# Kernel tuning notes

Hardware: AMD Instinct MI355X
Metric: run time of the kernel (lower is better)

## Reference

```python
import jax, jax.numpy as jnp
import numpy as np

KH = KW = 9
BN_EPS = 1e-5


def conv3x3(x, w):
    # x: [B,Cin,H,W], w: [Cout,Cin,3,3], stride 1, padding 1
    return jax.lax.conv_general_dilated(
        x, w, window_strides=(1, 1), padding=((1, 1), (1, 1)),
        dimension_numbers=("NCHW", "OIHW", "NCHW"))


def cbr(x, w, bn):
    # bn: [4, C] rows = (gamma, beta, running_mean, running_var); inference-mode BN
    g, b, m, v = bn[0], bn[1], bn[2], bn[3]
    x = conv3x3(x, w)
    x = (x - m[:, None, None]) * (g[:, None, None] / jnp.sqrt(v[:, None, None] + BN_EPS)) + b[:, None, None]
    return jax.nn.relu(x)


def weighting(x, atten):
    # x: [B,C,H,W], atten: [B,H,W,KH*KW]
    # out[b,c,h,w] = sum_k atten[b,h,w,k] * x[b,c, h+dh(k), w+dw(k)]  (zero-padded window)
    B, C, H, W = x.shape
    patches = jax.lax.conv_general_dilated_patches(
        x, filter_shape=(KH, KW), window_strides=(1, 1),
        padding=((KH // 2, KH // 2), (KW // 2, KW // 2)))  # [B, C*KH*KW, H, W], channel-major
    patches = patches.reshape(B, C, KH * KW, H, W)
    return jnp.einsum("bckhw,bhwk->bchw", patches, atten)


def _make_params(key, fc_dim=1024):
    d4, d16 = fc_dim // 4, fc_dim // 16
    ks = jax.random.split(key, 16)
    def conv_w(k, co, ci):
        return jax.random.normal(k, (co, ci, 3, 3), jnp.float32) * (1.0 / np.sqrt(ci * 9))
    def bn(k, c):
        g = 1.0 + 0.1 * jax.random.normal(k, (c,), jnp.float32)
        return jnp.stack([g, jnp.zeros((c,)), jnp.zeros((c,)), jnp.ones((c,))])
    p = {}
    p["w1"], p["bn1"] = conv_w(ks[0], d4, fc_dim), bn(ks[1], d4)
    p["w2"], p["bn2"] = conv_w(ks[2], d16, d4), bn(ks[3], d16)
    p["w3"], p["bn3"] = conv_w(ks[4], d4, d16), bn(ks[5], d4)
    p["w4"], p["bn4"] = conv_w(ks[6], d4, fc_dim), bn(ks[7], d4)
    p["w5"], p["bn5"] = conv_w(ks[8], d4, d4), bn(ks[9], d4)
    p["fw1"] = jax.random.normal(ks[10], (10, d4), jnp.float32) * (1.0 / np.sqrt(d4))
    p["fb1"] = jnp.zeros((10,), jnp.float32)
    p["fw2"] = jax.random.normal(ks[11], (1, 10), jnp.float32) * (1.0 / np.sqrt(10))
    p["fb2"] = jnp.zeros((1,), jnp.float32)
    return p


def setup_inputs() -> dict:
    key = jax.random.key(0)
    k1, k2, k3, kp = jax.random.split(key, 4)
    B, fc_dim, H, W = 4, 1024, 64, 64
    inp = {
        "low_key": jax.random.normal(k1, (B, fc_dim, H, W), jnp.float32),
        "low_nonkey": jax.random.normal(k2, (B, fc_dim, H, W), jnp.float32),
        "local_atten": jax.random.uniform(k3, (B, H, W, KH * KW), jnp.float32),
    }
    inp.update(_make_params(kp, fc_dim))
    return inp


def reference(low_key, low_nonkey, local_atten,
              w1, bn1, w2, bn2, w3, bn3, w4, bn4, w5, bn5,
              fw1, fb1, fw2, fb2):
    x = cbr(low_key, w1, bn1)        # [B, 256, H, W]
    x = cbr(x, w2, bn2)              # [B, 64, H, W]
    x = weighting(x, local_atten)    # 9x9 local-attention weighted gather
    x = cbr(x, w3, bn3)              # [B, 256, H, W]
    y = cbr(low_nonkey, w4, bn4)     # [B, 256, H, W]
    out = cbr(x - y, w5, bn5)        # [B, 256, H, W]
    out = out.mean(axis=(2, 3))      # adaptive avg pool to 1x1 -> [B, 256]
    out = out @ fw1.T + fb1          # [B, 10]
    out = out @ fw2.T + fb2          # [B, 1]
    return out
```

## Files before the change

### kernel.cpp

```cpp
#include <hip/hip_runtime.h>
#include <math.h>

typedef _Float16 f16;
typedef f16 f16x4 __attribute__((ext_vector_type(4)));
typedef f16 f16x8 __attribute__((ext_vector_type(8)));
typedef float f32x4 __attribute__((ext_vector_type(4)));

#define NB 4

__global__ void __launch_bounds__(256)
wtrans_kernel(const float* __restrict__ w, f16* __restrict__ wt, int Co, int Cin) {
  int idx = blockIdx.x * 256 + threadIdx.x;
  int total = Co * Cin * 9;
  if (idx >= total) return;
  int ci = idx % Cin, t2 = idx / Cin;
  int co = t2 % Co, k = t2 / Co;
  wt[idx] = (f16)w[((size_t)co * Cin + ci) * 9 + k];
}

__global__ void __launch_bounds__(256)
nchw2nhwc(const float* __restrict__ in, f16* __restrict__ out) {
  __shared__ f16 s[64][66];
  const int t = threadIdx.x;
  const int bh = blockIdx.x, c0 = blockIdx.y * 64;
  const int b = bh >> 6, h = bh & 63;
  const int w = t & 63, cr = t >> 6;
  #pragma unroll
  for (int i = 0; i < 16; ++i) {
    int c = c0 + cr * 16 + i;
    s[cr * 16 + i][w] = (f16)in[(((size_t)b * 1024 + c) * 64 + h) * 64 + w];
  }
  __syncthreads();
  #pragma unroll
  for (int i = 0; i < 2; ++i) {
    int task = t + 256 * i;
    int oct = task & 7, w2 = task >> 3;
    f16x8 v;
    #pragma unroll
    for (int j = 0; j < 8; ++j) v[j] = s[oct * 8 + j][w2];
    *(f16x8*)(out + (((size_t)b * 64 + h) * 64 + w2) * 1024 + c0 + oct * 8) = v;
  }
}

__global__ void __launch_bounds__(256)
conv_mfma(const f16* __restrict__ in, const f16* __restrict__ in2,
          const f16* __restrict__ wt, const float* __restrict__ bn,
          f16* __restrict__ out, float* __restrict__ partial,
          int Cin, int Co) {
  __shared__ __align__(16) f16 xs[6][66][40];
  __shared__ __align__(16) f16 ws[9][64][32];
  __shared__ float s_red[4][64];

  const int t = threadIdx.x;
  const int tile = blockIdx.x;
  const int b = tile >> 4;
  const int h0 = (tile & 15) * 4;
  const int co_blk = blockIdx.y * 64;
  const int wid = t >> 6, lane = t & 63;
  const int l15 = lane & 15, lg = lane >> 4;
  const int koff = lg * 8;

  f32x4 acc[4][4];
  #pragma unroll
  for (int m = 0; m < 4; ++m)
    #pragma unroll
    for (int n = 0; n < 4; ++n)
      #pragma unroll
      for (int r = 0; r < 4; ++r) acc[m][n][r] = 0.f;

  const f16* inb = in + (size_t)b * Cin * 4096;
  const f16* inb2 = in2 ? in2 + (size_t)b * Cin * 4096 : nullptr;

  const int wS = t >> 2, octS = t & 3;
  const int NC = Cin >> 5;
  f16x8 ireg[6], wreg[9];

  auto load_stage = [&](int ci0) {
    #pragma unroll
    for (int r = 0; r < 6; ++r) {
      int gh = h0 - 1 + r;
      f16x8 v = {};
      if ((unsigned)gh < 64u) {
        size_t off = ((size_t)gh * 64 + wS) * Cin + ci0 + octS * 8;
        v = *(const f16x8*)(inb + off);
        if (inb2) { f16x8 v2 = *(const f16x8*)(inb2 + off); v = v - v2; }
      }
      ireg[r] = v;
    }
    #pragma unroll
    for (int i = 0; i < 9; ++i) {
      int s = t + 256 * i;
      int oct = s & 3, co = (s >> 2) & 63, k = s >> 8;
      wreg[i] = *(const f16x8*)(wt + ((size_t)k * Co + co_blk + co) * Cin + ci0 + oct * 8);
    }
  };
  auto write_stage = [&]() {
    #pragma unroll
    for (int r = 0; r < 6; ++r)
      *(f16x8*)&xs[r][wS + 1][octS * 8] = ireg[r];
    #pragma unroll
    for (int i = 0; i < 9; ++i) {
      int s = t + 256 * i;
      int oct = s & 3, co = (s >> 2) & 63, k = s >> 8;
      *(f16x8*)&ws[k][co][oct * 8] = wreg[i];
    }
  };

  if (t < 48) {
    int r = t >> 3, side = (t >> 2) & 1, oc = t & 3;
    f16x8 z = {};
    *(f16x8*)&xs[r][side * 65][oc * 8] = z;
  }
  load_stage(0);
  write_stage();
  __syncthreads();

  for (int c = 0; c < NC; ++c) {
    if (c + 1 < NC) load_stage((c + 1) << 5);
    #pragma unroll
    for (int tap = 0; tap < 9; ++tap) {
      const int dh = tap / 3 - 1, dw = tap % 3 - 1;
      f16x8 af[4];
      #pragma unroll
      for (int m = 0; m < 4; ++m)
        af[m] = *(const f16x8*)&ws[tap][m * 16 + l15][koff];
      #pragma unroll
      for (int n = 0; n < 4; ++n) {
        const f16x8 bf = *(const f16x8*)&xs[wid + dh + 1][n * 16 + l15 + 1 + dw][koff];
        #pragma unroll
        for (int m = 0; m < 4; ++m)
          acc[m][n] = __builtin_amdgcn_mfma_f32_16x16x32_f16(af[m], bf, acc[m][n], 0, 0, 0);
      }
    }
    __syncthreads();
    if (c + 1 < NC) write_stage();
    __syncthreads();
  }

  if (out) {
    #pragma unroll
    for (int m = 0; m < 4; ++m) {
      float sc[4], sh[4];
      #pragma unroll
      for (int reg = 0; reg < 4; ++reg) {
        int co = co_blk + m * 16 + lg * 4 + reg;
        sc[reg] = bn[co] / sqrtf(bn[3 * Co + co] + 1e-5f);
        sh[reg] = bn[Co + co] - bn[2 * Co + co] * sc[reg];
      }
      #pragma unroll
      for (int n = 0; n < 4; ++n) {
        f16x4 v;
        #pragma unroll
        for (int reg = 0; reg < 4; ++reg)
          v[reg] = (f16)fmaxf(fmaf(acc[m][n][reg], sc[reg], sh[reg]), 0.f);
        *(f16x4*)(out + ((size_t)(b * 64 + h0 + wid) * 64 + n * 16 + l15) * Co
                      + co_blk + m * 16 + lg * 4) = v;
      }
    }
  } else {
    #pragma unroll
    for (int m = 0; m < 4; ++m)
      #pragma unroll
      for (int reg = 0; reg < 4; ++reg) {
        int co = co_blk + m * 16 + lg * 4 + reg;
        float sc = bn[co] / sqrtf(bn[3 * Co + co] + 1e-5f);
        float sh = bn[Co + co] - bn[2 * Co + co] * sc;
        float s = 0.f;
        #pragma unroll
        for (int n = 0; n < 4; ++n)
          s += fmaxf(fmaf(acc[m][n][reg], sc, sh), 0.f);
        s += __shfl_xor(s, 1, 64);
        s += __shfl_xor(s, 2, 64);
        s += __shfl_xor(s, 4, 64);
        s += __shfl_xor(s, 8, 64);
        if (l15 == 0) s_red[wid][m * 16 + lg * 4 + reg] = s;
      }
    __syncthreads();
    if (t < 64) {
      float v = s_red[0][t] + s_red[1][t] + s_red[2][t] + s_red[3][t];
      partial[((size_t)b * Co + co_blk + t) * 16 + (tile & 15)] = v;
    }
  }
}

__global__ void __launch_bounds__(256)
weighting_nhwc(const f16* __restrict__ x, const float* __restrict__ atten,
               f16* __restrict__ out) {
  __shared__ float s_a[64 * 81];
  const int h = blockIdx.x, b = blockIdx.y;
  const int t = threadIdx.x;
  for (int idx = t; idx < 64 * 81; idx += 256)
    s_a[idx] = atten[(size_t)((b * 64 + h) * 64) * 81 + idx];
  __syncthreads();

  const int w = t & 63, cg = t >> 6;
  float acc[16];
  #pragma unroll
  for (int j = 0; j < 16; ++j) acc[j] = 0.f;

  for (int dh = -4; dh <= 4; ++dh) {
    int hh = h + dh;
    if ((unsigned)hh >= 64u) continue;
    #pragma unroll
    for (int dw = -4; dw <= 4; ++dw) {
      int ww = w + dw;
      if ((unsigned)ww >= 64u) continue;
      float a = s_a[w * 81 + (dh + 4) * 9 + (dw + 4)];
      const f16* xp = x + (((size_t)b * 64 + hh) * 64 + ww) * 64 + cg * 16;
      f16x8 v0 = *(const f16x8*)xp;
      f16x8 v1 = *(const f16x8*)(xp + 8);
      #pragma unroll
      for (int j = 0; j < 8; ++j) {
        acc[j]     = fmaf(a, (float)v0[j], acc[j]);
        acc[8 + j] = fmaf(a, (float)v1[j], acc[8 + j]);
      }
    }
  }
  f16x8 o0, o1;
  #pragma unroll
  for (int j = 0; j < 8; ++j) { o0[j] = (f16)acc[j]; o1[j] = (f16)acc[8 + j]; }
  f16* op = out + (((size_t)b * 64 + h) * 64 + w) * 64 + cg * 16;
  *(f16x8*)op = o0;
  *(f16x8*)(op + 8) = o1;
}

__global__ void __launch_bounds__(256)
fc_kernel(const float* __restrict__ partial, const float* __restrict__ fw1,
          const float* __restrict__ fb1, const float* __restrict__ fw2,
          const float* __restrict__ fb2, float* __restrict__ outp) {
  const int t = threadIdx.x;
  const int b = t >> 6, lane = t & 63;
  float pooled[4];
  #pragma unroll
  for (int k = 0; k < 4; ++k) {
    int c = lane + 64 * k;
    float s = 0.f;
    #pragma unroll
    for (int p = 0; p < 16; ++p) s += partial[(size_t)(b * 256 + c) * 16 + p];
    pooled[k] = s * (1.f / 4096.f);
  }
  float o = 0.f;
  for (int i = 0; i < 10; ++i) {
    float d = 0.f;
    #pragma unroll
    for (int k = 0; k < 4; ++k) d += pooled[k] * fw1[i * 256 + lane + 64 * k];
    #pragma unroll
    for (int off = 32; off > 0; off >>= 1) d += __shfl_down(d, off, 64);
    o += (d + fb1[i]) * fw2[i];
  }
  if (lane == 0) outp[b] = o + fb2[0];
}

extern "C" void kernel_launch(void* const* d_in, const int* in_sizes, int n_in,
                              void* d_out, int out_size, void* d_ws, size_t ws_size,
                              hipStream_t stream) {
  const float* low_key    = (const float*)d_in[0];
  const float* low_nonkey = (const float*)d_in[1];
  const float* atten      = (const float*)d_in[2];
  const float* w1 = (const float*)d_in[3];  const float* bn1 = (const float*)d_in[4];
  const float* w2 = (const float*)d_in[5];  const float* bn2 = (const float*)d_in[6];
  const float* w3 = (const float*)d_in[7];  const float* bn3 = (const float*)d_in[8];
  const float* w4 = (const float*)d_in[9];  const float* bn4 = (const float*)d_in[10];
  const float* w5 = (const float*)d_in[11]; const float* bn5 = (const float*)d_in[12];
  const float* fw1 = (const float*)d_in[13]; const float* fb1 = (const float*)d_in[14];
  const float* fw2 = (const float*)d_in[15]; const float* fb2 = (const float*)d_in[16];

  f16* T   = (f16*)d_ws;
  f16* X1  = T + 16777216;
  f16* X2  = X1 + 4194304;
  f16* X3  = X2 + 1048576;
  f16* Y   = X3 + 1048576;
  f16* wt1 = Y + 4194304;
  f16* wt2 = wt1 + 2359296;
  f16* wt3 = wt2 + 147456;
  f16* wt4 = wt3 + 147456;
  f16* wt5 = wt4 + 2359296;
  float* P = (float*)(wt5 + 589824);

  dim3 blk(256);
  wtrans_kernel<<<(256 * 1024 * 9 + 255) / 256, blk, 0, stream>>>(w1, wt1, 256, 1024);
  wtrans_kernel<<<(64 * 256 * 9 + 255) / 256, blk, 0, stream>>>(w2, wt2, 64, 256);
  wtrans_kernel<<<(256 * 64 * 9 + 255) / 256, blk, 0, stream>>>(w3, wt3, 256, 64);
  wtrans_kernel<<<(256 * 1024 * 9 + 255) / 256, blk, 0, stream>>>(w4, wt4, 256, 1024);
  wtrans_kernel<<<(256 * 256 * 9 + 255) / 256, blk, 0, stream>>>(w5, wt5, 256, 256);

  nchw2nhwc<<<dim3(256, 16), blk, 0, stream>>>(low_key, T);
  conv_mfma<<<dim3(64, 4), blk, 0, stream>>>(T, nullptr, wt1, bn1, X1, nullptr, 1024, 256);
  conv_mfma<<<dim3(64, 1), blk, 0, stream>>>(X1, nullptr, wt2, bn2, X2, nullptr, 256, 64);
  weighting_nhwc<<<dim3(64, NB), blk, 0, stream>>>(X2, atten, X3);
  conv_mfma<<<dim3(64, 4), blk, 0, stream>>>(X3, nullptr, wt3, bn3, X1, nullptr, 64, 256);
  nchw2nhwc<<<dim3(256, 16), blk, 0, stream>>>(low_nonkey, T);
  conv_mfma<<<dim3(64, 4), blk, 0, stream>>>(T, nullptr, wt4, bn4, Y, nullptr, 1024, 256);
  conv_mfma<<<dim3(64, 4), blk, 0, stream>>>(X1, Y, wt5, bn5, nullptr, P, 256, 256);
  fc_kernel<<<1, 256, 0, stream>>>(P, fw1, fb1, fw2, fb2, (float*)d_out);
}
```

Before: 326.7 us.

## Split-K the two 1024-channel convolutions and add an fp32 reduce kernel

The two large 1024-input-channel convolutions now split the input-channel reduction across two grid z-slices. Each slice writes fp32 partial accumulators to a workspace buffer, and a new kreduce kernel sums them and applies BN+ReLU to produce fp16 NHWC output. This doubles the block count from 256 to 512 to fill more CUs on the MI355X. The cost is an extra kernel launch and roughly 64MB of extra fp32 traffic per conv. The weight LDS tile is also padded from 32 to 40 halves to reduce bank conflicts.

```diff
diff --git a/kernel.cpp b/kernel.cpp
--- a/kernel.cpp
+++ b/kernel.cpp
@@ -45,10 +45,10 @@
 __global__ void __launch_bounds__(256)
 conv_mfma(const f16* __restrict__ in, const f16* __restrict__ in2,
           const f16* __restrict__ wt, const float* __restrict__ bn,
-          f16* __restrict__ out, float* __restrict__ partial,
-          int Cin, int Co) {
+          f16* __restrict__ out, float* __restrict__ pacc,
+          float* __restrict__ partial, int Cin, int Co, int kspl) {
   __shared__ __align__(16) f16 xs[6][66][40];
-  __shared__ __align__(16) f16 ws[9][64][32];
+  __shared__ __align__(16) f16 ws[9][64][40];
   __shared__ float s_red[4][64];
 
   const int t = threadIdx.x;
@@ -56,6 +56,8 @@
   const int b = tile >> 4;
   const int h0 = (tile & 15) * 4;
   const int co_blk = blockIdx.y * 64;
+  const int ciBase = blockIdx.z * (Cin / kspl);
+  const int NC = (Cin / kspl) >> 5;
   const int wid = t >> 6, lane = t & 63;
   const int l15 = lane & 15, lg = lane >> 4;
   const int koff = lg * 8;
@@ -72,7 +74,6 @@
   const f16* inb2 = in2 ? in2 + (size_t)b * Cin * 4096 : nullptr;
 
   const int wS = t >> 2, octS = t & 3;
-  const int NC = Cin >> 5;
   f16x8 ireg[6], wreg[9];
 
   auto load_stage = [&](int ci0) {
@@ -111,12 +112,12 @@
     f16x8 z = {};
     *(f16x8*)&xs[r][side * 65][oc * 8] = z;
   }
-  load_stage(0);
+  load_stage(ciBase);
   write_stage();
   __syncthreads();
 
   for (int c = 0; c < NC; ++c) {
-    if (c + 1 < NC) load_stage((c + 1) << 5);
+    if (c + 1 < NC) load_stage(ciBase + ((c + 1) << 5));
     #pragma unroll
     for (int tap = 0; tap < 9; ++tap) {
       const int dh = tap / 3 - 1, dw = tap % 3 - 1;
@@ -137,7 +138,16 @@
     __syncthreads();
   }
 
-  if (out) {
+  if (pacc) {
+    float* pb = pacc + (size_t)blockIdx.z * 4194304 + (size_t)b * 4096 * Co;
+    #pragma unroll
+    for (int m = 0; m < 4; ++m)
+      #pragma unroll
+      for (int n = 0; n < 4; ++n) {
+        int px = (h0 + wid) * 64 + n * 16 + l15;
+        *(f32x4*)(pb + (size_t)px * Co + co_blk + m * 16 + lg * 4) = acc[m][n];
+      }
+  } else if (out) {
     #pragma unroll
     for (int m = 0; m < 4; ++m) {
       float sc[4], sh[4];
@@ -184,6 +194,31 @@
 }
 
 __global__ void __launch_bounds__(256)
+kreduce(const float* __restrict__ pacc, const float* __restrict__ bn,
+        f16* __restrict__ out, int Co) {
+  const int t = threadIdx.x;
+  const int coq = t & 63;
+  float sc[4], sh[4];
+  #pragma unroll
+  for (int r = 0; r < 4; ++r) {
+    int co = coq * 4 + r;
+    sc[r] = bn[co] / sqrtf(bn[3 * Co + co] + 1e-5f);
+    sh[r] = bn[Co + co] - bn[2 * Co + co] * sc[r];
+  }
+  #pragma unroll
+  for (int i = 0; i < 4; ++i) {
+    size_t idx = (size_t)blockIdx.x * 1024 + i * 256 + t;
+    f32x4 a = *(const f32x4*)(pacc + idx * 4);
+    f32x4 b2 = *(const f32x4*)(pacc + 4194304 + idx * 4);
+    f16x4 v;
+    #pragma unroll
+    for (int r = 0; r < 4; ++r)
+      v[r] = (f16)fmaxf(fmaf(a[r] + b2[r], sc[r], sh[r]), 0.f);
+    *(f16x4*)(out + idx * 4) = v;
+  }
+}
+
+__global__ void __launch_bounds__(256)
 weighting_nhwc(const f16* __restrict__ x, const float* __restrict__ atten,
                f16* __restrict__ out) {
   __shared__ float s_a[64 * 81];
@@ -275,7 +310,8 @@
   f16* wt3 = wt2 + 147456;
   f16* wt4 = wt3 + 147456;
   f16* wt5 = wt4 + 2359296;
-  float* P = (float*)(wt5 + 589824);
+  float* P    = (float*)(wt5 + 589824);
+  float* Pacc = P + 16384;
 
   dim3 blk(256);
   wtrans_kernel<<<(256 * 1024 * 9 + 255) / 256, blk, 0, stream>>>(w1, wt1, 256, 1024);
@@ -285,12 +321,14 @@
   wtrans_kernel<<<(256 * 256 * 9 + 255) / 256, blk, 0, stream>>>(w5, wt5, 256, 256);
 
   nchw2nhwc<<<dim3(256, 16), blk, 0, stream>>>(low_key, T);
-  conv_mfma<<<dim3(64, 4), blk, 0, stream>>>(T, nullptr, wt1, bn1, X1, nullptr, 1024, 256);
-  conv_mfma<<<dim3(64, 1), blk, 0, stream>>>(X1, nullptr, wt2, bn2, X2, nullptr, 256, 64);
+  conv_mfma<<<dim3(64, 4, 2), blk, 0, stream>>>(T, nullptr, wt1, bn1, nullptr, Pacc, nullptr, 1024, 256, 2);
+  kreduce<<<1024, blk, 0, stream>>>(Pacc, bn1, X1, 256);
+  conv_mfma<<<dim3(64, 1, 1), blk, 0, stream>>>(X1, nullptr, wt2, bn2, X2, nullptr, nullptr, 256, 64, 1);
   weighting_nhwc<<<dim3(64, NB), blk, 0, stream>>>(X2, atten, X3);
-  conv_mfma<<<dim3(64, 4), blk, 0, stream>>>(X3, nullptr, wt3, bn3, X1, nullptr, 64, 256);
+  conv_mfma<<<dim3(64, 4, 1), blk, 0, stream>>>(X3, nullptr, wt3, bn3, X1, nullptr, nullptr, 64, 256, 1);
   nchw2nhwc<<<dim3(256, 16), blk, 0, stream>>>(low_nonkey, T);
-  conv_mfma<<<dim3(64, 4), blk, 0, stream>>>(T, nullptr, wt4, bn4, Y, nullptr, 1024, 256);
-  conv_mfma<<<dim3(64, 4), blk, 0, stream>>>(X1, Y, wt5, bn5, nullptr, P, 256, 256);
+  conv_mfma<<<dim3(64, 4, 2), blk, 0, stream>>>(T, nullptr, wt4, bn4, nullptr, Pacc, nullptr, 1024, 256, 2);
+  kreduce<<<1024, blk, 0, stream>>>(Pacc, bn4, Y, 256);
+  conv_mfma<<<dim3(64, 4, 1), blk, 0, stream>>>(X1, Y, wt5, bn5, nullptr, nullptr, P, 256, 256, 1);
   fc_kernel<<<1, 256, 0, stream>>>(P, fw1, fb1, fw2, fb2, (float*)d_out);
 }
```

New measurement: 337.6 us. 3.3% more time.
